# Kernel optimization log

Measured on AMD Instinct MI355X. Metric: run time of the kernel, lower is better.

Reference implementation:

```python
import jax, jax.numpy as jnp
import numpy as np

W_LEN = 8      # window_len
DEPTH = 3      # sig_depth (implementation hardcodes depth-3 truncated signature)


def _seg_exp(d):
    """Truncated tensor-exponential of a linear segment with increment d (N,D)."""
    t1 = d
    t2 = 0.5 * jnp.einsum('ni,nj->nij', d, d)
    t3 = jnp.einsum('nij,nk->nijk', t2, d) / 3.0  # d^{\otimes 3}/6
    return t1, t2, t3


def _signature_depth3(path):
    """path: (N, L, D) -> flattened depth-3 signature (N, D + D^2 + D^3),
    matching signatory.signature ordering (levels concatenated, row-major)."""
    N, L, D = path.shape
    dx = path[:, 1:] - path[:, :-1]          # (N, L-1, D) increments
    s1, s2, s3 = _seg_exp(dx[:, 0])

    def chen_step(carry, d):
        s1, s2, s3 = carry
        t1, t2, t3 = _seg_exp(d)
        n1 = s1 + t1
        n2 = s2 + jnp.einsum('ni,nj->nij', s1, t1) + t2
        n3 = (s3
              + jnp.einsum('nij,nk->nijk', s2, t1)
              + jnp.einsum('ni,njk->nijk', s1, t2)
              + t3)
        return (n1, n2, n3), None

    # scan over the remaining L-2 increments (time axis leading)
    (s1, s2, s3), _ = jax.lax.scan(chen_step, (s1, s2, s3),
                                   jnp.moveaxis(dx[:, 1:], 1, 0))
    return jnp.concatenate([s1, s2.reshape(N, -1), s3.reshape(N, -1)], axis=-1)


def _rolling_windows(x, w_len):
    """x: (B,T,D) -> (B,T,W,D); window t covers [max(0,t-W+1), t],
    left-padded by repeating the first element (clamped indices)."""
    T = x.shape[1]
    idx = jnp.clip(jnp.arange(T)[:, None] - (w_len - 1) + jnp.arange(w_len)[None, :], 0, T - 1)  # (T,W)
    return x[:, idx]  # (B,T,W,D)


def setup_inputs() -> dict:
    key = jax.random.key(0)
    k1, k2, k3 = jax.random.split(key, 3)
    B, T, D = 8, 4096, 8
    sig_channels = D + D * D + D * D * D  # 584
    proj_dim = 128
    x = jax.random.normal(k1, (B, T, D), dtype=jnp.float32)
    w_proj = jax.random.normal(k2, (sig_channels, proj_dim), dtype=jnp.float32) * (1.0 / np.sqrt(sig_channels))
    b_proj = jax.random.normal(k3, (proj_dim,), dtype=jnp.float32) * 0.01
    return {"x": x, "w_proj": w_proj, "b_proj": b_proj}


def reference(x, w_proj, b_proj):
    B, T, D = x.shape
    windows = _rolling_windows(x, W_LEN).reshape(B * T, W_LEN, D)
    sig = _signature_depth3(windows).reshape(B, T, -1)   # (B,T,584)
    return sig @ w_proj + b_proj                          # (B,T,128)
```

## Files before the change

### kernel.cpp

```cpp
#include <hip/hip_runtime.h>
#include <hip/hip_bf16.h>

typedef unsigned short ushort_t;
typedef __attribute__((ext_vector_type(8))) short short8;
typedef __attribute__((ext_vector_type(4))) float floatx4;
typedef __attribute__((ext_vector_type(4))) int intx4;

#define SIG_CH 584
#define KPAD   608
#define NPROJ  128
#define ASTRIDE 616
#define TLEN   4096
#define NWIN   32768
#define DROWS  4103
#define WPB    32

__device__ __forceinline__ ushort_t f2bf(float f) {
    unsigned int v; __builtin_memcpy(&v, &f, 4);
    v += 0x7fffu + ((v >> 16) & 1u);
    return (ushort_t)(v >> 16);
}

__device__ __forceinline__ ushort_t f2bf_hw(float f) {
    __hip_bfloat16 h = __float2bfloat16(f);
    ushort_t u; __builtin_memcpy(&u, &h, 2);
    return u;
}

#define W_THREADS   (KPAD * NPROJ)
#define D4_THREADS  (8 * DROWS * 2)
__global__ void pack_kernel(const float* __restrict__ w, const float* __restrict__ x,
                            ushort_t* __restrict__ wp, float* __restrict__ dincP) {
    int idx = blockIdx.x * 256 + threadIdx.x;
    if (idx < W_THREADS) {
        int n = idx & (NPROJ - 1);
        int c = idx >> 7;
        ushort_t v = 0;
        if (c < SIG_CH) v = f2bf(w[c * NPROJ + n]);
        wp[((size_t)(c >> 3) * NPROJ + n) * 8 + (c & 7)] = v;
        return;
    }
    int id2 = idx - W_THREADS;
    if (id2 >= D4_THREADS) return;
    int h  = id2 & 1;
    int rr = (id2 >> 1) % DROWS;
    int b  = (id2 >> 1) / DROWS;
    floatx4 v = floatx4{0.f, 0.f, 0.f, 0.f};
    if (rr >= 8) {
        int ta = rr - 8;
        const floatx4* xb4 = (const floatx4*)(x + (size_t)b * TLEN * 8);
        v = xb4[(ta + 1) * 2 + h] - xb4[ta * 2 + h];
    }
    ((floatx4*)dincP)[((size_t)b * DROWS + rr) * 2 + h] = v;
}

__launch_bounds__(256, 3)
__global__ void sig_gemm_kernel(const float* __restrict__ dincP,
                                const ushort_t* __restrict__ wp,
                                const float* __restrict__ bias,
                                float* __restrict__ out) {
    __shared__ __align__(16) float    s_dinc[WPB + 6][8];
    __shared__ __align__(16) ushort_t s_A[WPB][ASTRIDE];

    const int tid  = threadIdx.x;
    const int blk  = blockIdx.x;
    const int g0   = blk * WPB;
    const int b    = g0 >> 12;
    const int t0   = g0 & (TLEN - 1);
    const float* dincB = dincP + (size_t)b * DROWS * 8;

    if (tid < (WPB + 6) * 2) {
        ((floatx4*)s_dinc)[tid] =
            *(const floatx4*)(dincB + (size_t)(t0 + 1) * 8 + tid * 4);
    }
    for (int idx = tid; idx < WPB * 32; idx += 256) {
        int r = idx >> 5, c = SIG_CH + (idx & 31);
        s_A[r][c] = 0;
    }
    __syncthreads();

    const int wv   = tid >> 6;
    const int lane = tid & 63;
    const int li   = lane >> 3;
    const int lj   = lane & 7;

    #pragma unroll 1
    for (int wp2 = 0; wp2 < 4; ++wp2) {
        const int w = wv * 8 + wp2 * 2;
        const int  woff = __builtin_amdgcn_readfirstlane((t0 + 1 + w) * 8);
        const float* dwp = dincB + woff;

        float diL[8], djL[8];
        #pragma unroll
        for (int r = 0; r < 8; ++r) {
            diL[r] = s_dinc[w + r][li];
            djL[r] = s_dinc[w + r][lj];
        }

        float hA = 0.f, gA = 0.f, s2A = 0.f;
        float hB = 0.f, gB = 0.f, s2B = 0.f;
        float s3A[8] = {0.f,0.f,0.f,0.f,0.f,0.f,0.f,0.f};
        float s3B[8] = {0.f,0.f,0.f,0.f,0.f,0.f,0.f,0.f};

        #pragma unroll
        for (int st = 0; st < 7; ++st) {
            const float diA = diL[st],     djA = djL[st];
            const float diB = diL[st + 1], djB = djL[st + 1];
            const float c3A = fmaf(djA, fmaf(0.166666667f, diA, 0.5f * hA), s2A);
            const float c3B = fmaf(djB, fmaf(0.166666667f, diB, 0.5f * hB), s2B);
            s2A = fmaf(djA, fmaf(0.5f, diA, hA), s2A);
            s2B = fmaf(djB, fmaf(0.5f, diB, hB), s2B);
            #pragma unroll
            for (int k = 0; k < 8; ++k) {
                s3A[k] = fmaf(c3A, dwp[st * 8 + k],       s3A[k]);
                s3B[k] = fmaf(c3B, dwp[(st + 1) * 8 + k], s3B[k]);
            }
            hA += diA; gA += djA;
            hB += diB; gB += djB;
        }

        union { ushort_t u[8]; intx4 v; } pkA, pkB;
        #pragma unroll
        for (int k = 0; k < 8; k += 2) {
            __hip_bfloat162 a2 = __float22bfloat162_rn(float2{s3A[k], s3A[k + 1]});
            __hip_bfloat162 b2 = __float22bfloat162_rn(float2{s3B[k], s3B[k + 1]});
            __builtin_memcpy(&pkA.u[k], &a2, 4);
            __builtin_memcpy(&pkB.u[k], &b2, 4);
        }
        *(intx4*)(&s_A[w][72 + lane * 8])     = pkA.v;
        *(intx4*)(&s_A[w + 1][72 + lane * 8]) = pkB.v;
        s_A[w][8 + lane]     = f2bf_hw(s2A);
        s_A[w + 1][8 + lane] = f2bf_hw(s2B);
        if (lane < 8) {
            s_A[w][lane]     = f2bf_hw(gA);
            s_A[w + 1][lane] = f2bf_hw(gB);
        }
    }
    __syncthreads();

    const int lrow  = lane & 15;
    const int kgrp  = lane >> 4;
    const int ncol0 = wv * 32 + lrow;

    floatx4 acc[2][2];
    #pragma unroll
    for (int mt = 0; mt < 2; ++mt) {
        acc[mt][0] = floatx4{0.f, 0.f, 0.f, 0.f};
        acc[mt][1] = floatx4{0.f, 0.f, 0.f, 0.f};
    }

    for (int kc = 0; kc < 19; ++kc) {
        const int kb = kc * 4 + kgrp;
        const short8 b0 = *(const short8*)(wp + ((size_t)kb * NPROJ + ncol0) * 8);
        const short8 b1 = *(const short8*)(wp + ((size_t)kb * NPROJ + ncol0 + 16) * 8);
        #pragma unroll
        for (int mt = 0; mt < 2; ++mt) {
            const short8 af = *(const short8*)(&s_A[mt * 16 + lrow][kc * 32 + kgrp * 8]);
            acc[mt][0] = __builtin_amdgcn_mfma_f32_16x16x32_bf16(af, b0, acc[mt][0], 0, 0, 0);
            acc[mt][1] = __builtin_amdgcn_mfma_f32_16x16x32_bf16(af, b1, acc[mt][1], 0, 0, 0);
        }
    }

    const float bias0 = bias[ncol0];
    const float bias1 = bias[ncol0 + 16];
    #pragma unroll
    for (int mt = 0; mt < 2; ++mt) {
        #pragma unroll
        for (int r = 0; r < 4; ++r) {
            const int row = g0 + mt * 16 + kgrp * 4 + r;
            out[(size_t)row * NPROJ + ncol0]      = acc[mt][0][r] + bias0;
            out[(size_t)row * NPROJ + ncol0 + 16] = acc[mt][1][r] + bias1;
        }
    }
}

extern "C" void kernel_launch(void* const* d_in, const int* in_sizes, int n_in,
                              void* d_out, int out_size, void* d_ws, size_t ws_size,
                              hipStream_t stream) {
    const float* x  = (const float*)d_in[0];
    const float* w  = (const float*)d_in[1];
    const float* bp = (const float*)d_in[2];
    ushort_t* wp    = (ushort_t*)d_ws;
    float*    dincP = (float*)((char*)d_ws + 160 * 1024);
    float* out = (float*)d_out;

    const int prep_total = W_THREADS + D4_THREADS;
    hipLaunchKernelGGL(pack_kernel, dim3((prep_total + 255) / 256), dim3(256), 0, stream,
                       w, x, wp, dincP);
    hipLaunchKernelGGL(sig_gemm_kernel, dim3(NWIN / WPB), dim3(256), 0, stream,
                       dincP, wp, bp, out);
}
```

Before: 73.98 us.

## Compute path increments inside main kernel and read them from LDS

Removes the increment precompute pass from the prep kernel. The main kernel now computes clamped window increments directly from x while filling shared memory, and the s3 inner loop reads increments as float4 vectors from LDS instead of uniform global loads. The weight pack is also rewritten so each thread writes one 16-byte vector of eight bf16 values. This is meant to cut a workspace round trip, shrink the prep launch and avoid scalar global loads in the hot loop, at the cost of a little redundant subtraction per block.

```diff
diff --git a/kernel.cpp b/kernel.cpp
--- a/kernel.cpp
+++ b/kernel.cpp
@@ -12,7 +12,6 @@
 #define ASTRIDE 616
 #define TLEN   4096
 #define NWIN   32768
-#define DROWS  4103
 #define WPB    32
 
 __device__ __forceinline__ ushort_t f2bf(float f) {
@@ -27,35 +26,22 @@
     return u;
 }
 
-#define W_THREADS   (KPAD * NPROJ)
-#define D4_THREADS  (8 * DROWS * 2)
-__global__ void pack_kernel(const float* __restrict__ w, const float* __restrict__ x,
-                            ushort_t* __restrict__ wp, float* __restrict__ dincP) {
+__global__ void pack_w_kernel(const float* __restrict__ w, ushort_t* __restrict__ wp) {
     int idx = blockIdx.x * 256 + threadIdx.x;
-    if (idx < W_THREADS) {
-        int n = idx & (NPROJ - 1);
-        int c = idx >> 7;
-        ushort_t v = 0;
-        if (c < SIG_CH) v = f2bf(w[c * NPROJ + n]);
-        wp[((size_t)(c >> 3) * NPROJ + n) * 8 + (c & 7)] = v;
-        return;
+    if (idx >= (KPAD / 8) * NPROJ) return;
+    int n  = idx & (NPROJ - 1);
+    int kb = idx >> 7;
+    union { ushort_t u[8]; intx4 v; } pk;
+    #pragma unroll
+    for (int kk = 0; kk < 8; ++kk) {
+        int c = kb * 8 + kk;
+        pk.u[kk] = (c < SIG_CH) ? f2bf(w[c * NPROJ + n]) : (ushort_t)0;
     }
-    int id2 = idx - W_THREADS;
-    if (id2 >= D4_THREADS) return;
-    int h  = id2 & 1;
-    int rr = (id2 >> 1) % DROWS;
-    int b  = (id2 >> 1) / DROWS;
-    floatx4 v = floatx4{0.f, 0.f, 0.f, 0.f};
-    if (rr >= 8) {
-        int ta = rr - 8;
-        const floatx4* xb4 = (const floatx4*)(x + (size_t)b * TLEN * 8);
-        v = xb4[(ta + 1) * 2 + h] - xb4[ta * 2 + h];
-    }
-    ((floatx4*)dincP)[((size_t)b * DROWS + rr) * 2 + h] = v;
+    *(intx4*)(wp + ((size_t)kb * NPROJ + n) * 8) = pk.v;
 }
 
 __launch_bounds__(256, 3)
-__global__ void sig_gemm_kernel(const float* __restrict__ dincP,
+__global__ void sig_gemm_kernel(const float* __restrict__ x,
                                 const ushort_t* __restrict__ wp,
                                 const float* __restrict__ bias,
                                 float* __restrict__ out) {
@@ -67,11 +53,14 @@
     const int g0   = blk * WPB;
     const int b    = g0 >> 12;
     const int t0   = g0 & (TLEN - 1);
-    const float* dincB = dincP + (size_t)b * DROWS * 8;
 
     if (tid < (WPB + 6) * 2) {
-        ((floatx4*)s_dinc)[tid] =
-            *(const floatx4*)(dincB + (size_t)(t0 + 1) * 8 + tid * 4);
+        const int h = tid & 1, r = tid >> 1;
+        const int u  = t0 - 7 + r;
+        const int ua = u < 0 ? 0 : u;
+        const int ub = (u + 1) < 0 ? 0 : (u + 1);
+        const floatx4* xb4 = (const floatx4*)(x + ((size_t)b << 15));
+        ((floatx4*)s_dinc)[tid] = xb4[ub * 2 + h] - xb4[ua * 2 + h];
     }
     for (int idx = tid; idx < WPB * 32; idx += 256) {
         int r = idx >> 5, c = SIG_CH + (idx & 31);
@@ -87,8 +76,6 @@
     #pragma unroll 1
     for (int wp2 = 0; wp2 < 4; ++wp2) {
         const int w = wv * 8 + wp2 * 2;
-        const int  woff = __builtin_amdgcn_readfirstlane((t0 + 1 + w) * 8);
-        const float* dwp = dincB + woff;
 
         float diL[8], djL[8];
         #pragma unroll
@@ -102,8 +89,13 @@
         float s3A[8] = {0.f,0.f,0.f,0.f,0.f,0.f,0.f,0.f};
         float s3B[8] = {0.f,0.f,0.f,0.f,0.f,0.f,0.f,0.f};
 
+        floatx4 ra0 = *(const floatx4*)(&s_dinc[w][0]);
+        floatx4 ra1 = *(const floatx4*)(&s_dinc[w][4]);
+
         #pragma unroll
         for (int st = 0; st < 7; ++st) {
+            const floatx4 rb0 = *(const floatx4*)(&s_dinc[w + st + 1][0]);
+            const floatx4 rb1 = *(const floatx4*)(&s_dinc[w + st + 1][4]);
             const float diA = diL[st],     djA = djL[st];
             const float diB = diL[st + 1], djB = djL[st + 1];
             const float c3A = fmaf(djA, fmaf(0.166666667f, diA, 0.5f * hA), s2A);
@@ -111,12 +103,15 @@
             s2A = fmaf(djA, fmaf(0.5f, diA, hA), s2A);
             s2B = fmaf(djB, fmaf(0.5f, diB, hB), s2B);
             #pragma unroll
-            for (int k = 0; k < 8; ++k) {
-                s3A[k] = fmaf(c3A, dwp[st * 8 + k],       s3A[k]);
-                s3B[k] = fmaf(c3B, dwp[(st + 1) * 8 + k], s3B[k]);
+            for (int k = 0; k < 4; ++k) {
+                s3A[k]     = fmaf(c3A, ra0[k], s3A[k]);
+                s3A[k + 4] = fmaf(c3A, ra1[k], s3A[k + 4]);
+                s3B[k]     = fmaf(c3B, rb0[k], s3B[k]);
+                s3B[k + 4] = fmaf(c3B, rb1[k], s3B[k + 4]);
             }
             hA += diA; gA += djA;
             hB += diB; gB += djB;
+            ra0 = rb0; ra1 = rb1;
         }
 
         union { ushort_t u[8]; intx4 v; } pkA, pkB;
@@ -181,12 +176,11 @@
     const float* w  = (const float*)d_in[1];
     const float* bp = (const float*)d_in[2];
     ushort_t* wp    = (ushort_t*)d_ws;
-    float*    dincP = (float*)((char*)d_ws + 160 * 1024);
     float* out = (float*)d_out;
 
-    const int prep_total = W_THREADS + D4_THREADS;
-    hipLaunchKernelGGL(pack_kernel, dim3((prep_total + 255) / 256), dim3(256), 0, stream,
-                       w, x, wp, dincP);
+    const int wpk_total = (KPAD / 8) * NPROJ;
+    hipLaunchKernelGGL(pack_w_kernel, dim3((wpk_total + 255) / 256), dim3(256), 0, stream,
+                       w, wp);
     hipLaunchKernelGGL(sig_gemm_kernel, dim3(NWIN / WPB), dim3(256), 0, stream,
-                       dincP, wp, bp, out);
+                       x, wp, bp, out);
 }
```

New measurement: 75.80 us. 2.5% more time.
